# Performance work log

Hardware: AMD Instinct MI355X
Metric: run time of the kernel (lower is better)

## Reference

```python
import jax, jax.numpy as jnp
import numpy as np

NUM_HEADS = 16

def _apply_rope(x, cos, sin):
    # x: (B, H, T, D); cos/sin: (T, D//2)
    B, H, T, D = x.shape
    xr = x.reshape(B, H, T, D // 2, 2)
    x0, x1 = xr[..., 0], xr[..., 1]
    c = cos[None, None, :, :]
    s = sin[None, None, :, :]
    out = jnp.stack([x0 * c - x1 * s, x0 * s + x1 * c], axis=-1)
    return out.reshape(B, H, T, D)


def setup_inputs() -> dict:
    key = jax.random.key(0)
    k1, k2, k3 = jax.random.split(key, 3)
    B, T, C = 2, 2048, 1024
    D = C // NUM_HEADS
    x = jax.random.normal(k1, (B, T, C), dtype=jnp.float32)
    qkv_w = jax.random.normal(k2, (3 * C, C), dtype=jnp.float32) * (C ** -0.5)
    proj_w = jax.random.normal(k3, (C, C), dtype=jnp.float32) * (C ** -0.5)
    # standard RoPE frequency table (theta = 10000)
    inv_freq = 1.0 / (10000.0 ** (jnp.arange(0, D, 2, dtype=jnp.float32) / D))  # (D/2,)
    angles = jnp.arange(T, dtype=jnp.float32)[:, None] * inv_freq[None, :]      # (T, D/2)
    return {
        "x": x,
        "freqs_cos": jnp.cos(angles),
        "freqs_sin": jnp.sin(angles),
        "qkv_w": qkv_w,
        "proj_w": proj_w,
    }


def reference(x, freqs_cos, freqs_sin, qkv_w, proj_w):
    B, T, C = x.shape
    H = NUM_HEADS
    D = C // H
    qkv = x @ qkv_w.T                                  # (B, T, 3C)
    q, k, v = jnp.split(qkv, 3, axis=-1)
    q = q.reshape(B, T, H, D).transpose(0, 2, 1, 3)    # (B, H, T, D)
    k = k.reshape(B, T, H, D).transpose(0, 2, 1, 3)
    v = v.reshape(B, T, H, D).transpose(0, 2, 1, 3)
    q = _apply_rope(q, freqs_cos, freqs_sin)
    k = _apply_rope(k, freqs_cos, freqs_sin)
    scale = 1.0 / jnp.sqrt(jnp.asarray(D, dtype=x.dtype))
    scores = jnp.einsum('bhqd,bhkd->bhqk', q, k) * scale
    causal = jnp.tril(jnp.ones((T, T), dtype=bool))
    scores = jnp.where(causal[None, None], scores, jnp.finfo(scores.dtype).min)
    attn = jax.nn.softmax(scores, axis=-1)
    out = jnp.einsum('bhqk,bhkd->bhqd', attn, v)       # (B, H, T, D)
    out = out.transpose(0, 2, 1, 3).reshape(B, T, C)
    return out @ proj_w.T
```

## Files before the change

### kernel.cpp

```cpp
#include <hip/hip_runtime.h>
#include <stdint.h>

#define DI __device__ __forceinline__

typedef unsigned short u16;
typedef __bf16 bf16x8 __attribute__((ext_vector_type(8)));
typedef unsigned short u16x8 __attribute__((ext_vector_type(8)));
typedef unsigned short u16x4 __attribute__((ext_vector_type(4)));
typedef float f32x4 __attribute__((ext_vector_type(4)));

DI u16 f2bf(float f) { __bf16 h = (__bf16)f; return __builtin_bit_cast(u16, h); }
DI float bf2f(u16 u) { return (float)__builtin_bit_cast(__bf16, u); }

DI bf16x8 ld8(const u16* p) { return __builtin_bit_cast(bf16x8, *(const u16x8*)p); }

DI f32x4 mfma16(bf16x8 a, bf16x8 b, f32x4 c) {
  return __builtin_amdgcn_mfma_f32_16x16x32_bf16(a, b, c, 0, 0, 0);
}

DI void async16(const u16* g, u16* l) {
  __builtin_amdgcn_global_load_lds((const __attribute__((address_space(1))) void*)g,
                                   (__attribute__((address_space(3))) void*)l, 16, 0, 0);
}

__global__ __launch_bounds__(256) void cast_all(const float* __restrict__ x,
                                                const float* __restrict__ qw,
                                                const float* __restrict__ pw,
                                                u16* __restrict__ xb, u16* __restrict__ qwb,
                                                u16* __restrict__ pwb) {
  const int bi = blockIdx.x;
  const float* src;
  u16* dst;
  int off;
  if (bi < 4096) {
    src = x; dst = xb; off = bi;
  } else if (bi < 7168) {
    src = qw; dst = qwb; off = bi - 4096;
  } else {
    src = pw; dst = pwb; off = bi - 7168;
  }
  const int i = off * 256 + threadIdx.x;
  const float4 v = ((const float4*)src)[i];
  u16x4 o = {f2bf(v.x), f2bf(v.y), f2bf(v.z), f2bf(v.w)};
  ((u16x4*)dst)[i] = o;
}

template <int OUT_BF16>
__global__ __launch_bounds__(256) void gemm_bt(const u16* __restrict__ A,
                                               const u16* __restrict__ W,
                                               void* __restrict__ outp,
                                               int M, int N, int K) {
  __shared__ u16 sA[2 * 4096];
  __shared__ u16 sB[2 * 4096];
  const int tid = threadIdx.x;
  const int w = tid >> 6, L = tid & 63;
  const int lo = L & 15, quad = L >> 4;
  const int nb = N >> 7;
  const int bm = blockIdx.x / nb, bn = blockIdx.x - bm * nb;
  const int m0 = bm << 7, n0 = bn << 7;
  const int wm = (w >> 1) << 6, wn = (w & 1) << 6;

  f32x4 acc[4][4];
#pragma unroll
  for (int i = 0; i < 4; ++i)
#pragma unroll
    for (int j = 0; j < 4; ++j) acc[i][j] = 0.f;

  const int r0 = tid >> 2, s0 = tid & 3;
  const int c0 = s0 ^ ((r0 >> 1) & 3);
  const int r1 = r0 + 64;
  const int c1 = s0 ^ ((r1 >> 1) & 3);
  const u16* aP0 = A + (size_t)(m0 + r0) * K + c0 * 8;
  const u16* aP1 = A + (size_t)(m0 + r1) * K + c1 * 8;
  const u16* bP0 = W + (size_t)(n0 + r0) * K + c0 * 8;
  const u16* bP1 = W + (size_t)(n0 + r1) * K + c1 * 8;
  u16* ldA0 = &sA[tid * 8];
  u16* ldA1 = &sA[(tid + 256) * 8];
  u16* ldB0 = &sB[tid * 8];
  u16* ldB1 = &sB[(tid + 256) * 8];

  int raf[4], rbf[4];
#pragma unroll
  for (int mt = 0; mt < 4; ++mt) {
    int r = wm + mt * 16 + lo;
    raf[mt] = r * 32 + ((quad ^ ((r >> 1) & 3)) << 3);
    r = wn + mt * 16 + lo;
    rbf[mt] = r * 32 + ((quad ^ ((r >> 1) & 3)) << 3);
  }

  auto stage = [&](int buf) {
    const int bo = buf << 12;
    async16(aP0, ldA0 + bo);
    async16(aP1, ldA1 + bo);
    async16(bP0, ldB0 + bo);
    async16(bP1, ldB1 + bo);
    aP0 += 32; aP1 += 32; bP0 += 32; bP1 += 32;
  };

  const int kIters = K >> 5;
  stage(0);
  for (int kt = 0; kt < kIters; ++kt) {
    __syncthreads();
    if (kt + 1 < kIters) stage((kt + 1) & 1);
    const int bo = (kt & 1) << 12;
    bf16x8 af[4], bfr[4];
#pragma unroll
    for (int mt = 0; mt < 4; ++mt) af[mt] = ld8(&sA[bo + raf[mt]]);
#pragma unroll
    for (int nt = 0; nt < 4; ++nt) bfr[nt] = ld8(&sB[bo + rbf[nt]]);
#pragma unroll
    for (int mt = 0; mt < 4; ++mt)
#pragma unroll
      for (int nt = 0; nt < 4; ++nt)
        acc[mt][nt] = mfma16(af[mt], bfr[nt], acc[mt][nt]);
  }

#pragma unroll
  for (int mt = 0; mt < 4; ++mt) {
    const int m = m0 + wm + mt * 16 + quad * 4;
#pragma unroll
    for (int nt = 0; nt < 4; ++nt) {
      const int n = n0 + wn + nt * 16 + lo;
#pragma unroll
      for (int r = 0; r < 4; ++r) {
        const size_t off = (size_t)(m + r) * N + n;
        if (OUT_BF16)
          ((u16*)outp)[off] = f2bf(acc[mt][nt][r]);
        else
          ((float*)outp)[off] = acc[mt][nt][r];
      }
    }
  }
}

#define QSCALE 0.18033688011112f
__global__ __launch_bounds__(256) void ropevt_k(const u16* __restrict__ qkv,
                                                const float* __restrict__ cosb,
                                                const float* __restrict__ sinb,
                                                u16* __restrict__ qo, u16* __restrict__ ko,
                                                u16* __restrict__ vto) {
  __shared__ u16 sT[64 * 64];
  const int tid = threadIdx.x;
  if (blockIdx.x < 8192) {
    const int idx = blockIdx.x * 256 + tid;
    const int i = idx & 31;
    const int t = (idx >> 5) & 2047;
    const int h = (idx >> 16) & 15;
    const int b = idx >> 20;
    const size_t src = ((size_t)(b * 2048 + t)) * 3072 + h * 64 + 2 * i;
    const float q0v = bf2f(qkv[src]), q1v = bf2f(qkv[src + 1]);
    const float k0v = bf2f(qkv[src + 1024]), k1v = bf2f(qkv[src + 1025]);
    const float c = cosb[t * 32 + i], s = sinb[t * 32 + i];
    const size_t dst = ((size_t)((b * 16 + h) * 2048 + t)) * 64 + 2 * i;
    qo[dst] = f2bf((q0v * c - q1v * s) * QSCALE);
    qo[dst + 1] = f2bf((q0v * s + q1v * c) * QSCALE);
    ko[dst] = f2bf(k0v * c - k1v * s);
    ko[dst + 1] = f2bf(k0v * s + k1v * c);
  } else {
    const int bi = blockIdx.x - 8192;
    const int bh = bi & 31;
    const int t0 = (bi >> 5) << 6;
    const int b = bh >> 4, h = bh & 15;
#pragma unroll
    for (int it = 0; it < 2; ++it) {
      const int id = tid + it * 256;
      const int tr = id >> 3, s = id & 7, c = s ^ (tr & 7);
      async16(qkv + (size_t)(b * 2048 + t0 + tr) * 3072 + 2048 + h * 64 + c * 8, &sT[id * 8]);
    }
    __syncthreads();
#pragma unroll
    for (int it = 0; it < 2; ++it) {
      const int id = tid + it * 256;
      const int d = id >> 3, ct = id & 7;
      u16x8 o;
#pragma unroll
      for (int j = 0; j < 8; ++j) {
        const int t = ct * 8 + j;
        o[j] = sT[t * 64 + (((d >> 3) ^ (t & 7)) << 3) + (d & 7)];
      }
      *(u16x8*)(vto + ((size_t)bh * 64 + d) * 2048 + t0 + ct * 8) = o;
    }
  }
}

__global__ __launch_bounds__(256) void fattn_part(const u16* __restrict__ qs,
                                                  const u16* __restrict__ ks,
                                                  const u16* __restrict__ vtb,
                                                  u16* __restrict__ opart,
                                                  float* __restrict__ lbuf) {
  __shared__ u16 sK[2 * 4096];
  __shared__ u16 sVt[2 * 4096];
  __shared__ u16 sP[4][16 * 64];
  const int tid = threadIdx.x;
  const int w = tid >> 6, L = tid & 63;
  const int lo = L & 15, quad = L >> 4;
  const int raw = blockIdx.x;
  const int part = raw & 1;
  const int bh = (raw >> 1) & 31;
  const int qi = 31 - (raw >> 6);
  const int n = qi + 1;
  const int h0 = (n + 1) >> 1;
  const int tk0 = part ? h0 : 0;
  const int tk1 = part ? n : h0;
  const size_t hoff = (size_t)bh * (2048 * 64);
  const int wq = (qi << 6) + w * 16;
  u16* sPw = sP[w];

  const int kvA = tid >> 3, cA = (tid & 7) ^ (kvA & 7);
  const int idB = tid + 256;
  const int kvB = idB >> 3, cB = (idB & 7) ^ (kvB & 7);
  const u16* kP0 = ks + hoff + (size_t)(tk0 * 64 + kvA) * 64 + cA * 8;
  const u16* kP1 = ks + hoff + (size_t)(tk0 * 64 + kvB) * 64 + cB * 8;
  const u16* vP0 = vtb + hoff + (size_t)kvA * 2048 + tk0 * 64 + cA * 8;
  const u16* vP1 = vtb + hoff + (size_t)kvB * 2048 + tk0 * 64 + cB * 8;
  u16* ldK0 = &sK[tid * 8];
  u16* ldK1 = &sK[idB * 8];
  u16* ldV0 = &sVt[tid * 8];
  u16* ldV1 = &sVt[idB * 8];

  auto stage = [&](int buf) {
    const int bo = buf << 12;
    async16(kP0, ldK0 + bo);
    async16(kP1, ldK1 + bo);
    async16(vP0, ldV0 + bo);
    async16(vP1, ldV1 + bo);
    kP0 += 4096; kP1 += 4096; vP0 += 64; vP1 += 64;
  };

  int kaOff[4][2], pOff[2], pwOff[4];
#pragma unroll
  for (int mt = 0; mt < 4; ++mt) {
    const int kv = mt * 16 + lo;
#pragma unroll
    for (int kd = 0; kd < 2; ++kd) {
      const int c = kd * 4 + quad;
      kaOff[mt][kd] = kv * 64 + ((c ^ (kv & 7)) << 3);
    }
    const int c2 = 2 * mt + (quad >> 1);
    pwOff[mt] = lo * 64 + ((c2 ^ (lo & 7)) << 3) + (quad & 1) * 4;
  }
#pragma unroll
  for (int kh = 0; kh < 2; ++kh) pOff[kh] = lo * 64 + (((kh * 4 + quad) ^ (lo & 7)) << 3);

  bf16x8 qb[2];
#pragma unroll
  for (int kd = 0; kd < 2; ++kd)
    qb[kd] = ld8(qs + hoff + (size_t)(wq + lo) * 64 + kd * 32 + quad * 8);

  bf16x8 ones;
#pragma unroll
  for (int j = 0; j < 8; ++j) ones[j] = (__bf16)1.0f;

  f32x4 lacc = 0.f;
  f32x4 ot[4];
#pragma unroll
  for (int mt = 0; mt < 4; ++mt) ot[mt] = 0.f;

  const int ntk = tk1 - tk0;
  if (ntk > 0) stage(0);
  for (int it2 = 0; it2 < ntk; ++it2) {
    __syncthreads();
    if (it2 + 1 < ntk) stage((it2 + 1) & 1);
    const int bo = (it2 & 1) << 12;
    const int kt = tk0 + it2;

    f32x4 st[4];
#pragma unroll
    for (int mt = 0; mt < 4; ++mt) st[mt] = 0.f;
#pragma unroll
    for (int mt = 0; mt < 4; ++mt)
#pragma unroll
      for (int kd = 0; kd < 2; ++kd)
        st[mt] = mfma16(ld8(&sK[bo + kaOff[mt][kd]]), qb[kd], st[mt]);

    if (kt == qi) {
      const int qg = wq + lo;
      const int kv0 = kt << 6;
#pragma unroll
      for (int mt = 0; mt < 4; ++mt)
#pragma unroll
        for (int r = 0; r < 4; ++r) {
          const int kvg = kv0 + mt * 16 + quad * 4 + r;
          if (kvg > qg) st[mt][r] = -3.0e38f;
        }
    }
#pragma unroll
    for (int mt = 0; mt < 4; ++mt) {
      u16x4 pk = {f2bf(__builtin_amdgcn_exp2f(st[mt][0])),
                  f2bf(__builtin_amdgcn_exp2f(st[mt][1])),
                  f2bf(__builtin_amdgcn_exp2f(st[mt][2])),
                  f2bf(__builtin_amdgcn_exp2f(st[mt][3]))};
      *(u16x4*)&sPw[pwOff[mt]] = pk;
    }
    asm volatile("s_waitcnt lgkmcnt(0)" ::: "memory");
    bf16x8 pbf[2];
#pragma unroll
    for (int kh = 0; kh < 2; ++kh) pbf[kh] = ld8(&sPw[pOff[kh]]);
    lacc = mfma16(ones, pbf[0], lacc);
    lacc = mfma16(ones, pbf[1], lacc);
#pragma unroll
    for (int mt = 0; mt < 4; ++mt)
#pragma unroll
      for (int kh = 0; kh < 2; ++kh)
        ot[mt] = mfma16(ld8(&sVt[bo + kaOff[mt][kh]]), pbf[kh], ot[mt]);
  }

  const int pq = bh * 32 + qi;
  u16* obase = opart + (size_t)(part * 1024 + pq) * 4096 + (size_t)(w * 16 + lo) * 64;
#pragma unroll
  for (int mt = 0; mt < 4; ++mt) {
    const int d0 = mt * 16 + quad * 4;
    u16x4 ok = {f2bf(ot[mt][0]), f2bf(ot[mt][1]), f2bf(ot[mt][2]), f2bf(ot[mt][3])};
    *(u16x4*)&obase[d0] = ok;
  }
  if (quad == 0) lbuf[(size_t)(part * 1024 + pq) * 64 + w * 16 + lo] = lacc[0];
}

__global__ __launch_bounds__(256) void fattn_merge(const u16* __restrict__ opart,
                                                   const float* __restrict__ lbuf,
                                                   u16* __restrict__ aout) {
  const int pq = blockIdx.x;
  const int bh = pq >> 5, qi = pq & 31;
  const int b = bh >> 4, h = bh & 15;
  const int tid = threadIdx.x;
#pragma unroll
  for (int it = 0; it < 2; ++it) {
    const int idx = tid + it * 256;
    const int q = idx >> 3, d0 = (idx & 7) * 8;
    const float l0 = lbuf[(size_t)pq * 64 + q];
    const float l1 = lbuf[(size_t)(1024 + pq) * 64 + q];
    const float inv = 1.f / (l0 + l1);
    const u16x8 o0 = *(const u16x8*)&opart[(size_t)pq * 4096 + q * 64 + d0];
    const u16x8 o1 = *(const u16x8*)&opart[(size_t)(1024 + pq) * 4096 + q * 64 + d0];
    u16x8 o;
#pragma unroll
    for (int j = 0; j < 8; ++j) o[j] = f2bf((bf2f(o0[j]) + bf2f(o1[j])) * inv);
    *(u16x8*)&aout[((size_t)(b * 2048 + qi * 64 + q)) * 1024 + h * 64 + d0] = o;
  }
}

extern "C" void kernel_launch(void* const* d_in, const int* in_sizes, int n_in,
                              void* d_out, int out_size, void* d_ws, size_t ws_size,
                              hipStream_t stream) {
  const float* x = (const float*)d_in[0];
  const float* fcos = (const float*)d_in[1];
  const float* fsin = (const float*)d_in[2];
  const float* qkvw = (const float*)d_in[3];
  const float* projw = (const float*)d_in[4];
  float* out = (float*)d_out;

  char* ws = (char*)d_ws;
  u16* x_bf = (u16*)(ws);
  u16* qkvw_bf = (u16*)(ws + (8u << 20));
  u16* projw_bf = (u16*)(ws + (14u << 20));
  u16* qkv_bf = (u16*)(ws + (16u << 20));
  u16* q_bf = (u16*)(ws + (40u << 20));
  u16* k_bf = (u16*)(ws + (48u << 20));
  u16* vt = (u16*)(ws + (56u << 20));
  u16* attn_bf = (u16*)(ws + (64u << 20));
  u16* opart = (u16*)(ws + (16u << 20));
  float* lbuf = (float*)(ws + (32u << 20));

  cast_all<<<8192, 256, 0, stream>>>(x, qkvw, projw, x_bf, qkvw_bf, projw_bf);
  gemm_bt<1><<<768, 256, 0, stream>>>(x_bf, qkvw_bf, (void*)qkv_bf, 4096, 3072, 1024);
  ropevt_k<<<9216, 256, 0, stream>>>(qkv_bf, fcos, fsin, q_bf, k_bf, vt);
  fattn_part<<<2048, 256, 0, stream>>>(q_bf, k_bf, vt, opart, lbuf);
  fattn_merge<<<1024, 256, 0, stream>>>(opart, lbuf, attn_bf);
  gemm_bt<0><<<256, 256, 0, stream>>>(attn_bf, projw_bf, (void*)out, 4096, 1024, 1024);
}
```

Measured before the change: 190.0 us.

## Fuse split-attention merge into output projection GEMM A-operand loading

Removes the separate fattn_merge kernel and its bf16 attention-output buffer. The projection GEMM now reads the two partial attention outputs and their softmax denominators straight from the workspace, combines and normalizes them in registers, and writes the result into shared memory as the A tile. This saves one launch and a full write-then-read of the intermediate activation. In exchange, the A tile is loaded synchronously through registers instead of async global-to-LDS copies, and the ALU merge work runs inside the GEMM main loop with a prefetch one step ahead.

```diff
diff --git a/kernel.cpp b/kernel.cpp
--- a/kernel.cpp
+++ b/kernel.cpp
@@ -45,10 +45,9 @@
   ((u16x4*)dst)[i] = o;
 }
 
-template <int OUT_BF16>
 __global__ __launch_bounds__(256) void gemm_bt(const u16* __restrict__ A,
                                                const u16* __restrict__ W,
-                                               void* __restrict__ outp,
+                                               u16* __restrict__ outp,
                                                int M, int N, int K) {
   __shared__ u16 sA[2 * 4096];
   __shared__ u16 sB[2 * 4096];
@@ -122,13 +121,7 @@
     for (int nt = 0; nt < 4; ++nt) {
       const int n = n0 + wn + nt * 16 + lo;
 #pragma unroll
-      for (int r = 0; r < 4; ++r) {
-        const size_t off = (size_t)(m + r) * N + n;
-        if (OUT_BF16)
-          ((u16*)outp)[off] = f2bf(acc[mt][nt][r]);
-        else
-          ((float*)outp)[off] = acc[mt][nt][r];
-      }
+      for (int r = 0; r < 4; ++r) outp[(size_t)(m + r) * N + n] = f2bf(acc[mt][nt][r]);
     }
   }
 }
@@ -316,26 +309,130 @@
   if (quad == 0) lbuf[(size_t)(part * 1024 + pq) * 64 + w * 16 + lo] = lacc[0];
 }
 
-__global__ __launch_bounds__(256) void fattn_merge(const u16* __restrict__ opart,
-                                                   const float* __restrict__ lbuf,
-                                                   u16* __restrict__ aout) {
-  const int pq = blockIdx.x;
-  const int bh = pq >> 5, qi = pq & 31;
-  const int b = bh >> 4, h = bh & 15;
+__global__ __launch_bounds__(256) void gemm_merge(const u16* __restrict__ opart,
+                                                  const float* __restrict__ lbuf,
+                                                  const u16* __restrict__ W,
+                                                  float* __restrict__ outp) {
+  constexpr int N = 1024, K = 1024;
+  __shared__ u16 sA[2 * 4096];
+  __shared__ u16 sB[2 * 4096];
   const int tid = threadIdx.x;
-#pragma unroll
-  for (int it = 0; it < 2; ++it) {
-    const int idx = tid + it * 256;
-    const int q = idx >> 3, d0 = (idx & 7) * 8;
-    const float l0 = lbuf[(size_t)pq * 64 + q];
-    const float l1 = lbuf[(size_t)(1024 + pq) * 64 + q];
-    const float inv = 1.f / (l0 + l1);
-    const u16x8 o0 = *(const u16x8*)&opart[(size_t)pq * 4096 + q * 64 + d0];
-    const u16x8 o1 = *(const u16x8*)&opart[(size_t)(1024 + pq) * 4096 + q * 64 + d0];
-    u16x8 o;
-#pragma unroll
-    for (int j = 0; j < 8; ++j) o[j] = f2bf((bf2f(o0[j]) + bf2f(o1[j])) * inv);
-    *(u16x8*)&aout[((size_t)(b * 2048 + qi * 64 + q)) * 1024 + h * 64 + d0] = o;
+  const int w = tid >> 6, L = tid & 63;
+  const int lo = L & 15, quad = L >> 4;
+  const int bm = blockIdx.x >> 3, bn = blockIdx.x & 7;
+  const int m0 = bm << 7, n0 = bn << 7;
+  const int wm = (w >> 1) << 6, wn = (w & 1) << 6;
+
+  f32x4 acc[4][4];
+#pragma unroll
+  for (int i = 0; i < 4; ++i)
+#pragma unroll
+    for (int j = 0; j < 4; ++j) acc[i][j] = 0.f;
+
+  const int r0 = tid >> 2, s0 = tid & 3;
+  const int c0 = s0 ^ ((r0 >> 1) & 3);
+  const int r1 = r0 + 64;
+  const int c1 = s0 ^ ((r1 >> 1) & 3);
+
+  const u16* bP0 = W + (size_t)(n0 + r0) * K + c0 * 8;
+  const u16* bP1 = W + (size_t)(n0 + r1) * K + c1 * 8;
+  u16* ldA0 = &sA[tid * 8];
+  u16* ldA1 = &sA[(tid + 256) * 8];
+  u16* ldB0 = &sB[tid * 8];
+  u16* ldB1 = &sB[(tid + 256) * 8];
+
+  const int m_0 = m0 + r0, m_1 = m0 + r1;
+  const int pqb0 = (m_0 >> 11) * 512 + ((m_0 & 2047) >> 6);
+  const int pqb1 = (m_1 >> 11) * 512 + ((m_1 & 2047) >> 6);
+  const int q_0 = m_0 & 63, q_1 = m_1 & 63;
+  const u16* oA0 = opart + (size_t)pqb0 * 4096 + q_0 * 64 + c0 * 8;
+  const u16* oB0 = oA0 + (size_t)1024 * 4096;
+  const u16* oA1 = opart + (size_t)pqb1 * 4096 + q_1 * 64 + c1 * 8;
+  const u16* oB1 = oA1 + (size_t)1024 * 4096;
+  const float* lq0 = lbuf + pqb0 * 64 + q_0;
+  const float* lq1 = lbuf + pqb1 * 64 + q_1;
+
+  u16x8 pr00, pr01, pr10, pr11;
+  float pl0a, pl0b, pl1a, pl1b;
+
+  auto fetchA = [&](int kt) {
+    const size_t off = ((size_t)(kt >> 1) << 17) + (size_t)((kt & 1) << 5);
+    pr00 = *(const u16x8*)(oA0 + off);
+    pr01 = *(const u16x8*)(oB0 + off);
+    pr10 = *(const u16x8*)(oA1 + off);
+    pr11 = *(const u16x8*)(oB1 + off);
+    if ((kt & 1) == 0) {
+      const int lh = (kt >> 1) * 2048;
+      pl0a = lq0[lh];
+      pl0b = lq0[lh + 65536];
+      pl1a = lq1[lh];
+      pl1b = lq1[lh + 65536];
+    }
+  };
+  auto commitA = [&](int buf) {
+    const int bo = buf << 12;
+    const float inv0 = 1.f / (pl0a + pl0b);
+    const float inv1 = 1.f / (pl1a + pl1b);
+    u16x8 a0, a1;
+#pragma unroll
+    for (int j = 0; j < 8; ++j) {
+      a0[j] = f2bf((bf2f(pr00[j]) + bf2f(pr01[j])) * inv0);
+      a1[j] = f2bf((bf2f(pr10[j]) + bf2f(pr11[j])) * inv1);
+    }
+    *(u16x8*)(ldA0 + bo) = a0;
+    *(u16x8*)(ldA1 + bo) = a1;
+  };
+  auto stageB = [&](int buf) {
+    const int bo = buf << 12;
+    async16(bP0, ldB0 + bo);
+    async16(bP1, ldB1 + bo);
+    bP0 += 32;
+    bP1 += 32;
+  };
+
+  int raf[4], rbf[4];
+#pragma unroll
+  for (int mt = 0; mt < 4; ++mt) {
+    int r = wm + mt * 16 + lo;
+    raf[mt] = r * 32 + ((quad ^ ((r >> 1) & 3)) << 3);
+    r = wn + mt * 16 + lo;
+    rbf[mt] = r * 32 + ((quad ^ ((r >> 1) & 3)) << 3);
+  }
+
+  stageB(0);
+  fetchA(0);
+  commitA(0);
+
+  const int kIters = K >> 5;
+  for (int kt = 0; kt < kIters; ++kt) {
+    __syncthreads();
+    if (kt + 1 < kIters) {
+      stageB((kt + 1) & 1);
+      fetchA(kt + 1);
+    }
+    const int bo = (kt & 1) << 12;
+    bf16x8 af[4], bfr[4];
+#pragma unroll
+    for (int mt = 0; mt < 4; ++mt) af[mt] = ld8(&sA[bo + raf[mt]]);
+#pragma unroll
+    for (int nt = 0; nt < 4; ++nt) bfr[nt] = ld8(&sB[bo + rbf[nt]]);
+#pragma unroll
+    for (int mt = 0; mt < 4; ++mt)
+#pragma unroll
+      for (int nt = 0; nt < 4; ++nt)
+        acc[mt][nt] = mfma16(af[mt], bfr[nt], acc[mt][nt]);
+    if (kt + 1 < kIters) commitA((kt + 1) & 1);
+  }
+
+#pragma unroll
+  for (int mt = 0; mt < 4; ++mt) {
+    const int m = m0 + wm + mt * 16 + quad * 4;
+#pragma unroll
+    for (int nt = 0; nt < 4; ++nt) {
+      const int n = n0 + wn + nt * 16 + lo;
+#pragma unroll
+      for (int r = 0; r < 4; ++r) outp[(size_t)(m + r) * N + n] = acc[mt][nt][r];
+    }
   }
 }
 
@@ -357,14 +454,12 @@
   u16* q_bf = (u16*)(ws + (40u << 20));
   u16* k_bf = (u16*)(ws + (48u << 20));
   u16* vt = (u16*)(ws + (56u << 20));
-  u16* attn_bf = (u16*)(ws + (64u << 20));
   u16* opart = (u16*)(ws + (16u << 20));
   float* lbuf = (float*)(ws + (32u << 20));
 
   cast_all<<<8192, 256, 0, stream>>>(x, qkvw, projw, x_bf, qkvw_bf, projw_bf);
-  gemm_bt<1><<<768, 256, 0, stream>>>(x_bf, qkvw_bf, (void*)qkv_bf, 4096, 3072, 1024);
+  gemm_bt<<<768, 256, 0, stream>>>(x_bf, qkvw_bf, qkv_bf, 4096, 3072, 1024);
   ropevt_k<<<9216, 256, 0, stream>>>(qkv_bf, fcos, fsin, q_bf, k_bf, vt);
   fattn_part<<<2048, 256, 0, stream>>>(q_bf, k_bf, vt, opart, lbuf);
-  fattn_merge<<<1024, 256, 0, stream>>>(opart, lbuf, attn_bf);
-  gemm_bt<0><<<256, 256, 0, stream>>>(attn_bf, projw_bf, (void*)out, 4096, 1024, 1024);
-}
+  gemm_merge<<<256, 256, 0, stream>>>(opart, lbuf, projw_bf, out);
+}
```

Result: slower. 196.8 us (+3.6%).
